# Performance work log

Measured on AMD Instinct MI355X. Metric: run time of the kernel, lower is better.

Reference implementation:

```python
import jax, jax.numpy as jnp
from jax import lax
import numpy as np

B = 16; C1 = 96; H4 = 28; W4 = 64
FULL_H = 448; FULL_W = 1024
BACKWARP = 1.25   # fltBackwarp for intLevel=4
SCALE = 16.0      # 2**intLevel
MD = 4            # correlation max displacement -> (2*MD+1)**2 = 81 channels


def _lrelu(x):
    return jnp.where(x >= 0, x, 0.1 * x)


def _conv3(x, w, b):
    y = lax.conv_general_dilated(x, w, (1, 1), [(1, 1), (1, 1)],
                                 dimension_numbers=('NCHW', 'OIHW', 'NCHW'))
    return y + b[None, :, None, None]


def _deconv4s2(x, w, b):
    # PyTorch ConvTranspose2d(k=4, s=2, p=1); w has PyTorch layout (in, out, kH, kW)
    wt = jnp.transpose(w[:, :, ::-1, ::-1], (1, 0, 2, 3))  # flipped, (out, in, kH, kW)
    y = lax.conv_general_dilated(x, wt, (1, 1), [(2, 2), (2, 2)],
                                 lhs_dilation=(2, 2),
                                 dimension_numbers=('NCHW', 'OIHW', 'NCHW'))
    return y + b[None, :, None, None]


def _correlation(f1, f2):
    # Channel-mean cost volume over a (2*MD+1)^2 displacement window.
    b, c, h, w = f1.shape
    f2p = jnp.pad(f2, ((0, 0), (0, 0), (MD, MD), (MD, MD)))
    vols = [jnp.mean(f1 * f2p[:, :, dy:dy + h, dx:dx + w], axis=1)
            for dy in range(2 * MD + 1) for dx in range(2 * MD + 1)]
    return jnp.stack(vols, axis=1)  # [B, 81, H, W]


def _warp(feat, flow):
    # Bilinear backward warp with zero padding outside the image.
    b, c, h, w = feat.shape
    gy, gx = jnp.meshgrid(jnp.arange(h, dtype=feat.dtype),
                          jnp.arange(w, dtype=feat.dtype), indexing='ij')
    x = gx[None] + flow[:, 0]
    y = gy[None] + flow[:, 1]
    x0 = jnp.floor(x); y0 = jnp.floor(y)
    wx = x - x0; wy = y - y0
    feat_flat = feat.reshape(b, c, h * w)

    def gather(yi, xi):
        valid = ((yi >= 0) & (yi <= h - 1) & (xi >= 0) & (xi <= w - 1)).astype(feat.dtype)
        yc = jnp.clip(yi, 0, h - 1).astype(jnp.int32)
        xc = jnp.clip(xi, 0, w - 1).astype(jnp.int32)
        idx = (yc * w + xc).reshape(b, 1, h * w)
        g = jnp.take_along_axis(feat_flat, jnp.broadcast_to(idx, (b, c, h * w)), axis=2)
        return g.reshape(b, c, h, w) * valid[:, None]

    return (gather(y0, x0) * ((1 - wy) * (1 - wx))[:, None]
            + gather(y0, x0 + 1) * ((1 - wy) * wx)[:, None]
            + gather(y0 + 1, x0) * (wy * (1 - wx))[:, None]
            + gather(y0 + 1, x0 + 1) * (wy * wx)[:, None])


def _quat_to_mat(q):
    # (w, x, y, z) quaternion -> rotation matrix, pytorch3d convention.
    q = q / jnp.linalg.norm(q, axis=-1, keepdims=True)
    w, x, y, z = q[:, 0], q[:, 1], q[:, 2], q[:, 3]
    R = jnp.stack([
        1 - 2 * (y * y + z * z), 2 * (x * y - w * z),     2 * (x * z + w * y),
        2 * (x * y + w * z),     1 - 2 * (x * x + z * z), 2 * (y * z - w * x),
        2 * (x * z - w * y),     2 * (y * z + w * x),     1 - 2 * (x * x + y * y)
    ], axis=-1).reshape(-1, 3, 3)
    return R


def _rot_flow(R, K, Kinv, h, w):
    # Rotational flow: p' = K R K^{-1} p (homogeneous), flow = p'/z - p.
    gy, gx = jnp.meshgrid(jnp.arange(h, dtype=R.dtype),
                          jnp.arange(w, dtype=R.dtype), indexing='ij')
    p = jnp.stack([gx.ravel(), gy.ravel(), jnp.ones(h * w, dtype=R.dtype)], axis=0)  # [3, HW]
    M = jnp.einsum('ij,bjk,kl->bil', K, R, Kinv)  # [B,3,3]
    pp = jnp.einsum('bij,jn->bin', M, p)
    pp2 = pp[:, :2] / pp[:, 2:3]
    return (pp2 - p[None, :2]).reshape(-1, 2, h, w)


def setup_inputs():
    key = jax.random.key(0)
    ks = jax.random.split(key, 24)

    def rnd(i, shape, scale=1.0):
        return scale * jax.random.normal(ks[i], shape, dtype=jnp.float32)

    def wconv(i, cout, cin, k=3):
        return rnd(i, (cout, cin, k, k), (2.0 / (cin * k * k)) ** 0.5)

    K = np.array([[500.0, 0.0, FULL_W / 2.0],
                  [0.0, 500.0, FULL_H / 2.0],
                  [0.0, 0.0, 1.0]], dtype=np.float32)
    quat = jnp.concatenate([jnp.ones((B, 1), jnp.float32), 0.01 * rnd(0, (B, 3))], axis=1)
    return {
        'tenOne': rnd(1, (B, C1, H4, W4)),
        'tenTwo': rnd(2, (B, C1, H4, W4)),
        'prev_flow': rnd(3, (B, 2, H4 // 2, W4 // 2)),
        'prev_feat': rnd(4, (B, 663, H4 // 2, W4 // 2)),
        'rotation_quat': quat,
        'cam_intri': jnp.asarray(K),
        'cam_intri_inv': jnp.asarray(np.linalg.inv(K)),
        'upflow_w': rnd(5, (2, 2, 4, 4), 0.1),
        'upflow_b': jnp.zeros((2,), jnp.float32),
        'upfeat_w': rnd(6, (663, 2, 4, 4), 0.02),
        'upfeat_b': jnp.zeros((2,), jnp.float32),
        'w1': wconv(7, 128, 183), 'b1': jnp.zeros((128,), jnp.float32),
        'w2': wconv(8, 128, 311), 'b2': jnp.zeros((128,), jnp.float32),
        'w3': wconv(9, 96, 439),  'b3': jnp.zeros((96,), jnp.float32),
        'w4': wconv(10, 64, 535), 'b4': jnp.zeros((64,), jnp.float32),
        'w5': wconv(11, 32, 599), 'b5': jnp.zeros((32,), jnp.float32),
        'w6': wconv(12, 2, 631),  'b6': jnp.zeros((2,), jnp.float32),
        'height': FULL_H,
        'width': FULL_W,
    }


def reference(tenOne, tenTwo, prev_flow, prev_feat, rotation_quat, cam_intri, cam_intri_inv,
              upflow_w, upflow_b, upfeat_w, upfeat_b,
              w1, b1, w2, b2, w3, b3, w4, b4, w5, b5, w6, b6, height, width):
    rh, rw = height // 16, width // 16  # 2**intLevel = 16
    delt_R = _quat_to_mat(rotation_quat)
    R_flow = _rot_flow(delt_R, cam_intri, cam_intri_inv, height, width)
    R_flow_r = jax.image.resize(R_flow, (R_flow.shape[0], 2, rh, rw), method='bilinear') / SCALE
    tenTwo_w = _warp(tenTwo, R_flow_r)
    tenFlow = _deconv4s2(prev_flow, upflow_w, upflow_b)
    tenFeatUp = _deconv4s2(prev_feat, upfeat_w, upfeat_b)
    tenVolume = _lrelu(_correlation(tenOne, _warp(tenTwo_w, tenFlow * BACKWARP)))
    feat = jnp.concatenate([tenVolume, R_flow_r, tenOne, tenFlow, tenFeatUp], axis=1)  # 183 ch
    for wc, bc in ((w1, b1), (w2, b2), (w3, b3), (w4, b4), (w5, b5)):
        feat = jnp.concatenate([_lrelu(_conv3(feat, wc, bc)), feat], axis=1)
    tenFlow_out = _lrelu(_conv3(feat, w6, b6))
    return tenFlow_out, feat
```

## Files before the change

### kernel.cpp

```cpp
#include <hip/hip_runtime.h>
#include <cstdint>
#include <cstddef>

typedef unsigned short u16;
typedef __attribute__((ext_vector_type(8))) short  short8;
typedef __attribute__((ext_vector_type(4))) float  f32x4;

#define HW4   1792
#define FCH   631
#define OUTOFF ((size_t)57344)

__device__ __forceinline__ float b2f(u16 u){
  union { unsigned int i; float f; } v; v.i = ((unsigned int)u) << 16; return v.f;
}
__device__ __forceinline__ u16 f2b(float f){
  unsigned int x = __float_as_uint(f);
  return (u16)((x + 0x7fffu + ((x >> 16) & 1u)) >> 16);
}
__device__ __forceinline__ float lrelu(float v){ return v >= 0.f ? v : 0.1f * v; }
__device__ __forceinline__ bool is_f32(const void* probe){ return ((const float*)probe)[0] > 1.0f; }
__device__ __forceinline__ float ldg_(const void* p, size_t i, bool f){
  return f ? ((const float*)p)[i] : b2f(((const u16*)p)[i]);
}
__device__ __forceinline__ void stg_(void* p, size_t i, float v, bool f){
  if (f) ((float*)p)[i] = v; else ((u16*)p)[i] = f2b(v);
}
__device__ __forceinline__ short8 zero8(){
  union { long long l[2]; short8 s; } z; z.l[0] = 0; z.l[1] = 0; return z.s;
}
__device__ __forceinline__ f32x4 zero4(){
  union { long long l[2]; f32x4 s; } z; z.l[0] = 0; z.l[1] = 0; return z.s;
}
__device__ __forceinline__ short8 swap16(short8 v){
  union { short8 s; unsigned int u[4]; } a, r;
  a.s = v;
  #pragma unroll
  for (int i = 0; i < 4; i++) r.u[i] = (a.u[i] >> 16) | (a.u[i] << 16);
  return r.s;
}

__global__ void k_M(const void* __restrict__ quat, const void* __restrict__ K,
                    const void* __restrict__ Kinv, float* __restrict__ Mout){
  bool f = is_f32(K);
  int b = threadIdx.x;
  if (b >= 16) return;
  float q0 = ldg_(quat,b*4+0,f), q1 = ldg_(quat,b*4+1,f);
  float q2 = ldg_(quat,b*4+2,f), q3 = ldg_(quat,b*4+3,f);
  float n = sqrtf(q0*q0 + q1*q1 + q2*q2 + q3*q3);
  float w = q0/n, x = q1/n, y = q2/n, z = q3/n;
  float R[9];
  R[0] = 1.f - 2.f*(y*y + z*z); R[1] = 2.f*(x*y - w*z); R[2] = 2.f*(x*z + w*y);
  R[3] = 2.f*(x*y + w*z); R[4] = 1.f - 2.f*(x*x + z*z); R[5] = 2.f*(y*z - w*x);
  R[6] = 2.f*(x*z - w*y); R[7] = 2.f*(y*z + w*x); R[8] = 1.f - 2.f*(x*x + y*y);
  float Kf[9], Ki[9];
  for (int i = 0; i < 9; i++){ Kf[i] = ldg_(K,i,f); Ki[i] = ldg_(Kinv,i,f); }
  float T[9];
  for (int r = 0; r < 3; r++)
    for (int c = 0; c < 3; c++)
      T[r*3+c] = R[r*3+0]*Ki[0*3+c] + R[r*3+1]*Ki[1*3+c] + R[r*3+2]*Ki[2*3+c];
  for (int r = 0; r < 3; r++)
    for (int c = 0; c < 3; c++)
      Mout[b*9 + r*3 + c] = Kf[r*3+0]*T[0*3+c] + Kf[r*3+1]*T[1*3+c] + Kf[r*3+2]*T[2*3+c];
}

__global__ void k_rflow_col(const float* __restrict__ Mws, float* __restrict__ tmpA){
  int t = blockIdx.x * 256 + threadIdx.x;
  int xo = t & 63;
  int yf = (t >> 6) % 448;
  int b  = t / (448*64);
  const float* M = Mws + b*9;
  float m0=M[0],m1=M[1],m2=M[2],m3=M[3],m4=M[4],m5=M[5],m6=M[6],m7=M[7],m8=M[8];
  float cx = 16.f*xo + 7.5f;
  float yff = (float)yf;
  float su = 0.f, sv = 0.f, wsum = 0.f;
  for (int i = 0; i < 32; i++){
    int xi = 16*xo - 8 + i;
    if (xi < 0 || xi > 1023) continue;
    float xf = (float)xi;
    float wgt = 1.f - fabsf(xf - cx) * (1.f/16.f);
    float den = m6*xf + m7*yff + m8;
    float inv = 1.f / den;
    float u = (m0*xf + m1*yff + m2)*inv - xf;
    float v = (m3*xf + m4*yff + m5)*inv - yff;
    su += wgt*u; sv += wgt*v; wsum += wgt;
  }
  float rn = 1.f / wsum;
  tmpA[((size_t)(b*2+0)*64 + xo)*448 + yf] = su*rn;
  tmpA[((size_t)(b*2+1)*64 + xo)*448 + yf] = sv*rn;
}

__global__ void k_rflow_row(const float* __restrict__ tmpA, float* __restrict__ rfr,
                            void* __restrict__ outb, const void* probe){
  bool f = is_f32(probe);
  int t = blockIdx.x * 256 + threadIdx.x;
  int xo = t & 63;
  int yo = (t >> 6) % 28;
  int b  = t / HW4;
  float cy = 16.f*yo + 7.5f;
  for (int c = 0; c < 2; c++){
    const float* col = tmpA + ((size_t)(b*2+c)*64 + xo)*448;
    float s = 0.f, wsum = 0.f;
    for (int i = 0; i < 32; i++){
      int yi = 16*yo - 8 + i;
      if (yi < 0 || yi > 447) continue;
      float wgt = 1.f - fabsf((float)yi - cy) * (1.f/16.f);
      s += wgt * col[yi]; wsum += wgt;
    }
    float val = s / (wsum * 16.0f);
    rfr[(size_t)(b*2+c)*HW4 + yo*64 + xo] = val;
    stg_(outb, OUTOFF + ((size_t)b*FCH + 529 + c)*HW4 + yo*64 + xo, val, f);
  }
}

__global__ void k_dflow(const void* __restrict__ pf, const void* __restrict__ w,
                        const void* __restrict__ bias, float* __restrict__ tflow,
                        void* __restrict__ outb, const void* probe){
  bool f = is_f32(probe);
  int t = blockIdx.x * 256 + threadIdx.x;
  int x = t & 63;
  int y = (t >> 6) % 28;
  int co = (t / HW4) & 1;
  int b  = t / (2*HW4);
  float acc = ldg_(bias, co, f);
  for (int ky = 0; ky < 4; ky++){
    int dy = y + ky - 2;
    if (dy < 0 || dy > 26 || (dy & 1)) continue;
    int iy = dy >> 1;
    for (int kx = 0; kx < 4; kx++){
      int dx = x + kx - 2;
      if (dx < 0 || dx > 62 || (dx & 1)) continue;
      int ix = dx >> 1;
      for (int ci = 0; ci < 2; ci++){
        acc += ldg_(pf, ((size_t)(b*2+ci)*14 + iy)*32 + ix, f) *
               ldg_(w,  (size_t)ci*32 + co*16 + (3-ky)*4 + (3-kx), f);
      }
    }
  }
  tflow[(size_t)(b*2+co)*HW4 + y*64 + x] = acc;
  stg_(outb, OUTOFF + ((size_t)b*FCH + 627 + co)*HW4 + y*64 + x, acc, f);
}

__global__ __launch_bounds__(512) void k_dfeat(
    const void* __restrict__ pfeat, const void* __restrict__ w,
    const void* __restrict__ bias, void* __restrict__ outb, const void* probe){
  bool f = is_f32(probe);
  __shared__ float red[8*128];
  int tid = threadIdx.x;
  int x = tid & 63;
  int s = tid >> 6;
  int b = blockIdx.x / 28;
  int y = blockIdx.x % 28;

  int iy0 = -1, iy1 = -1, wy0 = 0, wy1 = 0;
  {
    int n = 0;
    for (int ky = (y & 1); ky < 4; ky += 2){
      int dy = y + ky - 2;
      if (dy >= 0 && dy <= 26){
        if (n == 0){ iy0 = dy >> 1; wy0 = (3-ky)*4; }
        else       { iy1 = dy >> 1; wy1 = (3-ky)*4; }
        n++;
      }
    }
  }
  int ix0 = -1, ix1 = -1, wx0 = 0, wx1 = 0;
  {
    int n = 0;
    for (int kx = (x & 1); kx < 4; kx += 2){
      int dx = x + kx - 2;
      if (dx >= 0 && dx <= 62){
        if (n == 0){ ix0 = dx >> 1; wx0 = 3-kx; }
        else       { ix1 = dx >> 1; wx1 = 3-kx; }
        n++;
      }
    }
  }
  const bool v00 = (iy0 >= 0) && (ix0 >= 0);
  const bool v01 = (iy0 >= 0) && (ix1 >= 0);
  const bool v10 = (iy1 >= 0) && (ix0 >= 0);
  const bool v11 = (iy1 >= 0) && (ix1 >= 0);
  const int wo00 = wy0 + wx0, wo01 = wy0 + wx1, wo10 = wy1 + wx0, wo11 = wy1 + wx1;

  float acc0 = 0.f, acc1 = 0.f;
  const size_t pbase = (size_t)b * 663 * 448;
  const int ci_end = min(663, (s + 1) * 83);
  #pragma unroll 2
  for (int ci = s * 83; ci < ci_end; ci++){
    const size_t cbase = pbase + (size_t)ci * 448;
    const int wb = ci * 32;
    if (v00){ float iv = ldg_(pfeat, cbase + iy0*32 + ix0, f);
      acc0 += iv * ldg_(w, wb + wo00, f); acc1 += iv * ldg_(w, wb + 16 + wo00, f); }
    if (v01){ float iv = ldg_(pfeat, cbase + iy0*32 + ix1, f);
      acc0 += iv * ldg_(w, wb + wo01, f); acc1 += iv * ldg_(w, wb + 16 + wo01, f); }
    if (v10){ float iv = ldg_(pfeat, cbase + iy1*32 + ix0, f);
      acc0 += iv * ldg_(w, wb + wo10, f); acc1 += iv * ldg_(w, wb + 16 + wo10, f); }
    if (v11){ float iv = ldg_(pfeat, cbase + iy1*32 + ix1, f);
      acc0 += iv * ldg_(w, wb + wo11, f); acc1 += iv * ldg_(w, wb + 16 + wo11, f); }
  }
  red[s*128 + x]      = acc0;
  red[s*128 + 64 + x] = acc1;
  __syncthreads();
  if (tid < 128){
    int co = tid >> 6, xx = tid & 63;
    float t = ldg_(bias, co, f);
    #pragma unroll
    for (int q = 0; q < 8; q++) t += red[q*128 + co*64 + xx];
    stg_(outb, OUTOFF + ((size_t)b*FCH + 629 + co)*HW4 + y*64 + xx, t, f);
  }
}

__global__ void k_copy_one(const void* __restrict__ one, void* __restrict__ outb,
                           const void* probe){
  bool f = is_f32(probe);
  int t = blockIdx.x * 256 + threadIdx.x;
  int p = t % HW4;
  int c = (t / HW4) % 96;
  int b = t / (96*HW4);
  stg_(outb, OUTOFF + ((size_t)b*FCH + 531 + c)*HW4 + p,
       ldg_(one, (size_t)(b*96+c)*HW4 + p, f), f);
}

__global__ void k_warp2(const void* __restrict__ two, const float* __restrict__ rfr,
                        const float* __restrict__ tflow, float* __restrict__ wrp2,
                        const void* probe){
  bool f = is_f32(probe);
  int t = blockIdx.x * 256 + threadIdx.x;
  int x = t & 63;
  int y = (t >> 6) % 28;
  int c = (t / HW4) % 96;
  int b = t / (96*HW4);
  float qu = tflow[(size_t)(b*2+0)*HW4 + y*64 + x] * 1.25f;
  float qv = tflow[(size_t)(b*2+1)*HW4 + y*64 + x] * 1.25f;
  float qx = (float)x + qu, qy = (float)y + qv;
  float qx0 = floorf(qx), qy0 = floorf(qy);
  float wx = qx - qx0, wy = qy - qy0;
  const size_t cb = (size_t)(b*96+c)*HW4;
  float acc = 0.f;
  #pragma unroll
  for (int a = 0; a < 2; a++){
    #pragma unroll
    for (int bb = 0; bb < 2; bb++){
      float ry = qy0 + (float)a, rx = qx0 + (float)bb;
      if (ry < 0.f || ry > 27.f || rx < 0.f || rx > 63.f) continue;
      float W = (a ? wy : 1.f-wy) * (bb ? wx : 1.f-wx);
      int iry = (int)ry, irx = (int)rx;
      float su = rfr[(size_t)(b*2+0)*HW4 + iry*64 + irx];
      float sv = rfr[(size_t)(b*2+1)*HW4 + iry*64 + irx];
      float sx = rx + su, sy = ry + sv;
      float sx0 = floorf(sx), sy0 = floorf(sy);
      float swx = sx - sx0, swy = sy - sy0;
      float inner = 0.f;
      #pragma unroll
      for (int aa = 0; aa < 2; aa++){
        #pragma unroll
        for (int cc2 = 0; cc2 < 2; cc2++){
          float gy2 = sy0 + (float)aa, gx2 = sx0 + (float)cc2;
          if (gy2 < 0.f || gy2 > 27.f || gx2 < 0.f || gx2 > 63.f) continue;
          float wv = (aa ? swy : 1.f-swy) * (cc2 ? swx : 1.f-swx);
          inner += wv * ldg_(two, cb + (size_t)((int)gy2*64 + (int)gx2), f);
        }
      }
      acc += W * inner;
    }
  }
  wrp2[t] = acc;
}

__global__ void k_corr(const void* __restrict__ one, const float* __restrict__ two,
                       void* __restrict__ outb, const void* probe){
  bool f = is_f32(probe);
  int t = blockIdx.x * 256 + threadIdx.x;
  int x  = t & 63;
  int y  = (t >> 6) % 28;
  int dy = (t / HW4) % 9;
  int b  = t / (9*HW4);
  float acc[9];
  #pragma unroll
  for (int i = 0; i < 9; i++) acc[i] = 0.f;
  int row = y + dy - 4;
  if (row >= 0 && row < 28){
    for (int c = 0; c < 96; c++){
      float f1 = ldg_(one, (size_t)(b*96+c)*HW4 + y*64 + x, f);
      const float* rp = two + (size_t)(b*96+c)*HW4 + row*64;
      #pragma unroll
      for (int dx = 0; dx < 9; dx++){
        int xx = x + dx - 4;
        if (xx >= 0 && xx < 64) acc[dx] += f1 * rp[xx];
      }
    }
  }
  #pragma unroll
  for (int dx = 0; dx < 9; dx++){
    float v = lrelu(acc[dx] * (1.f/96.f));
    stg_(outb, OUTOFF + ((size_t)b*FCH + 448 + dy*9 + dx)*HW4 + y*64 + x, v, f);
  }
}

__global__ __launch_bounds__(256) void k_conv(
    void* __restrict__ base, size_t in_off,
    const void* __restrict__ w, const void* __restrict__ bias,
    int Cin, int Cout, size_t out_off, size_t out_bstr, const void* probe,
    int bf16_only){
  bool f = is_f32(probe);
  if (bf16_only && f) return;
  __shared__ float s_in[32*3*66];
  __shared__ float s_w[32*9*32];
  int tid = threadIdx.x;
  int x = tid & 63;
  int g = tid >> 6;
  int by = blockIdx.x;
  int b = by / 28, y = by % 28;
  int co_base = blockIdx.y * 32;
  const size_t FB = (size_t)FCH * HW4;
  float acc[8];
  #pragma unroll
  for (int j = 0; j < 8; j++) acc[j] = 0.f;

  for (int ci0 = 0; ci0 < Cin; ci0 += 32){
    int cc = min(32, Cin - ci0);
    if (f){
      const float* inb = (const float*)base + in_off + (size_t)b*FB;
      for (int e = tid; e < cc*198; e += 256){
        int ci = e / 198; int rem = e - ci*198;
        int r = rem / 66; int xx = rem - r*66;
        int iy = y + r - 1; int ix = xx - 1;
        float v = 0.f;
        if (iy >= 0 && iy < 28 && ix >= 0 && ix < 64)
          v = inb[(size_t)(ci0+ci)*HW4 + iy*64 + ix];
        s_in[(ci*3 + r)*66 + xx] = v;
      }
      const float* wf = (const float*)w;
      for (int e = tid; e < cc*288; e += 256){
        int co_i = e & 31; int k = (e >> 5) % 9; int ci = e / 288;
        int co = co_base + co_i;
        float v = 0.f;
        if (co < Cout) v = wf[((size_t)co*Cin + ci0 + ci)*9 + k];
        s_w[(ci*9 + k)*32 + co_i] = v;
      }
    } else {
      const u16* inb = (const u16*)base + in_off + (size_t)b*FB;
      for (int e = tid; e < cc*198; e += 256){
        int ci = e / 198; int rem = e - ci*198;
        int r = rem / 66; int xx = rem - r*66;
        int iy = y + r - 1; int ix = xx - 1;
        float v = 0.f;
        if (iy >= 0 && iy < 28 && ix >= 0 && ix < 64)
          v = b2f(inb[(size_t)(ci0+ci)*HW4 + iy*64 + ix]);
        s_in[(ci*3 + r)*66 + xx] = v;
      }
      const u16* wf = (const u16*)w;
      for (int e = tid; e < cc*288; e += 256){
        int co_i = e & 31; int k = (e >> 5) % 9; int ci = e / 288;
        int co = co_base + co_i;
        float v = 0.f;
        if (co < Cout) v = b2f(wf[((size_t)co*Cin + ci0 + ci)*9 + k]);
        s_w[(ci*9 + k)*32 + co_i] = v;
      }
    }
    __syncthreads();
    for (int ci = 0; ci < cc; ci++){
      const float* si = &s_in[ci*198 + x];
      const float* sw = &s_w[ci*288 + 8*g];
      #pragma unroll
      for (int ky = 0; ky < 3; ky++){
        #pragma unroll
        for (int kx = 0; kx < 3; kx++){
          float v = si[ky*66 + kx];
          const float* wp = sw + (ky*3 + kx)*32;
          float4 wa = *(const float4*)(wp);
          float4 wb = *(const float4*)(wp + 4);
          acc[0] += wa.x*v; acc[1] += wa.y*v; acc[2] += wa.z*v; acc[3] += wa.w*v;
          acc[4] += wb.x*v; acc[5] += wb.y*v; acc[6] += wb.z*v; acc[7] += wb.w*v;
        }
      }
    }
    __syncthreads();
  }
  #pragma unroll
  for (int j = 0; j < 8; j++){
    int co = co_base + 8*g + j;
    if (co < Cout){
      float v = lrelu(acc[j] + ldg_(bias, co, f));
      stg_(base, out_off + (size_t)b*out_bstr + (size_t)co*HW4 + y*64 + x, v, f);
    }
  }
}

__global__ void k_wprep(const void* __restrict__ w, u16* __restrict__ wT,
                        int Cin, int Cout, int nCB, int total, const void* probe){
  if (!is_f32(probe)) return;
  int t = blockIdx.x * 256 + threadIdx.x;
  if (t >= total) return;
  int j     = t & 7;
  int lane  = (t >> 3) & 63;
  int rest  = t >> 9;
  int tI    = rest & 3;
  int rest2 = rest >> 2;
  int tap   = rest2 % 9;
  int gc    = rest2 / 9;
  int cb    = gc % nCB;
  int gyb   = gc / nCB;
  int kk = ((lane >> 4) << 3) + j;
  int ci = cb*16 + (kk >> 1);
  int co = gyb*64 + tI*16 + (lane & 15);
  float x = 0.f;
  if (co < Cout && ci < Cin) x = ((const float*)w)[((size_t)co*Cin + ci)*9 + tap];
  u16 hi = f2b(x);
  wT[t] = (kk & 1) ? f2b(x - b2f(hi)) : hi;
}

__global__ __launch_bounds__(256, 2) void k_conv_ms(
    void* __restrict__ base, size_t in_off, const u16* __restrict__ wT,
    const void* __restrict__ bias, int Cin, int nCB, int Cout,
    size_t out_off, size_t out_bstr, const void* __restrict__ probe){
  if (!is_f32(probe)) return;
  __shared__ __align__(16) u16 lds[26624];
  const int tid  = threadIdx.x;
  const int lane = tid & 63, wv = tid >> 6;
  const int lx = lane & 15, lg = lane >> 4;
  const int wr  = wv & 1;
  const int wxh = wv >> 1;
  const int b  = blockIdx.x & 15;
  const int y0 = (blockIdx.x >> 4) * 2;
  const int coB = (int)blockIdx.y * 64;
  const float* inb = (const float*)base + in_off + (size_t)b * ((size_t)FCH * HW4);
  const u16* wTg = wT + (size_t)blockIdx.y * (size_t)nCB * 18432;

  f32x4 acc[4][2];
  #pragma unroll
  for (int tI = 0; tI < 4; tI++){ acc[tI][0] = zero4(); acc[tI][1] = zero4(); }

  int offb[3];
  #pragma unroll
  for (int kx = 0; kx < 3; kx++){
    int xo = lx + kx - 1;
    offb[kx] = (xo >> 4)*512 + (xo & 15)*32 + ((lg ^ ((xo >> 2) & 3)) << 3);
  }
  const bool maskB0 = (lx == 0  && wxh == 0);
  const bool maskB1 = (lx == 15 && wxh == 1);

  const int sx4 = tid & 15;
  const int sr  = (tid >> 4) & 3;
  const int srow = y0 - 1 + sr;
  const bool rok = (srow >= 0 && srow < 28);
  const int swz = sx4 & 3;
  const int nb0 = sr*64 + sx4*4;

  float4 paA[4], paB[4];
  short8 pwA[9], pwB[9];

  auto LOADA = [&](int cb){
    const u16* wsrc = wTg + (size_t)cb * 18432;
    #pragma unroll
    for (int i = 0; i < 9; i++)
      pwA[i] = *(const short8*)(wsrc + (size_t)(wv*9 + i)*512 + lane*8);
    #pragma unroll
    for (int i = 0; i < 4; i++){
      int ci = cb*16 + wv + 4*i;
      float4 v = {0.f, 0.f, 0.f, 0.f};
      if (rok && ci < Cin) v = *(const float4*)(inb + (size_t)ci*HW4 + srow*64 + sx4*4);
      paA[i] = v;
    }
  };
  auto LOADB = [&](int cb){
    const u16* wsrc = wTg + (size_t)cb * 18432;
    #pragma unroll
    for (int i = 0; i < 9; i++)
      pwB[i] = *(const short8*)(wsrc + (size_t)(wv*9 + i)*512 + lane*8);
    #pragma unroll
    for (int i = 0; i < 4; i++){
      int ci = cb*16 + wv + 4*i;
      float4 v = {0.f, 0.f, 0.f, 0.f};
      if (rok && ci < Cin) v = *(const float4*)(inb + (size_t)ci*HW4 + srow*64 + sx4*4);
      paB[i] = v;
    }
  };
  auto WRITEA = [&](){
    #pragma unroll
    for (int i = 0; i < 9; i++)
      *(short8*)&lds[8192 + (wv*9 + i)*512 + lane*8] = pwA[i];
    #pragma unroll
    for (int i = 0; i < 4; i++){
      int cil = wv + 4*i;
      int jo = (((cil >> 2) ^ swz) << 3) + 2*(cil & 3);
      #pragma unroll
      for (int u = 0; u < 4; u++){
        float xv = (&paA[i].x)[u];
        u16 hi = f2b(xv);
        u16 lo = f2b(xv - b2f(hi));
        *(unsigned int*)&lds[(nb0 + u)*32 + jo] = (unsigned int)hi | ((unsigned int)lo << 16);
      }
    }
  };
  auto WRITEB = [&](){
    #pragma unroll
    for (int i = 0; i < 9; i++)
      *(short8*)&lds[8192 + (wv*9 + i)*512 + lane*8] = pwB[i];
    #pragma unroll
    for (int i = 0; i < 4; i++){
      int cil = wv + 4*i;
      int jo = (((cil >> 2) ^ swz) << 3) + 2*(cil & 3);
      #pragma unroll
      for (int u = 0; u < 4; u++){
        float xv = (&paB[i].x)[u];
        u16 hi = f2b(xv);
        u16 lo = f2b(xv - b2f(hi));
        *(unsigned int*)&lds[(nb0 + u)*32 + jo] = (unsigned int)hi | ((unsigned int)lo << 16);
      }
    }
  };
  auto COMPUTE = [&](){
    #pragma unroll
    for (int ky = 0; ky < 3; ky++){
      const int rb = (wr + ky)*2048 + wxh*1024;
      #pragma unroll
      for (int kx = 0; kx < 3; kx++){
        const int k = ky*3 + kx;
        const int bA = rb + offb[kx];
        short8 B0 = *(const short8*)&lds[bA];
        short8 B1 = *(const short8*)&lds[bA + 512];
        if (kx == 0 && maskB0) B0 = zero8();
        if (kx == 2 && maskB1) B1 = zero8();
        short8 S0 = swap16(B0), S1 = swap16(B1);
        #pragma unroll
        for (int tI = 0; tI < 4; tI++){
          short8 Af = *(const short8*)&lds[8192 + ((k*4 + tI)*64 + lane)*8];
          acc[tI][0] = __builtin_amdgcn_mfma_f32_16x16x32_bf16(Af, B0, acc[tI][0], 0,0,0);
          acc[tI][0] = __builtin_amdgcn_mfma_f32_16x16x32_bf16(Af, S0, acc[tI][0], 0,0,0);
          acc[tI][1] = __builtin_amdgcn_mfma_f32_16x16x32_bf16(Af, B1, acc[tI][1], 0,0,0);
          acc[tI][1] = __builtin_amdgcn_mfma_f32_16x16x32_bf16(Af, S1, acc[tI][1], 0,0,0);
        }
      }
    }
  };

  LOADA(0);
  for (int cb = 0; cb < nCB; cb += 2){
    WRITEA();
    LOADB(cb + 1);
    __syncthreads();
    COMPUTE();
    __syncthreads();
    WRITEB();
    if (cb + 2 < nCB) LOADA(cb + 2);
    __syncthreads();
    COMPUTE();
    __syncthreads();
  }
  float* ob = (float*)base;
  const float* bf = (const float*)bias;
  const int y = y0 + wr;
  #pragma unroll
  for (int tI = 0; tI < 4; tI++){
    #pragma unroll
    for (int xg = 0; xg < 2; xg++){
      const int x = wxh*32 + xg*16 + lx;
      #pragma unroll
      for (int r4 = 0; r4 < 4; r4++){
        int co = coB + tI*16 + lg*4 + r4;
        if (co < Cout){
          float v = lrelu(acc[tI][xg][r4] + bf[co]);
          ob[out_off + (size_t)b*out_bstr + (size_t)co*HW4 + (size_t)(y*64 + x)] = v;
        }
      }
    }
  }
}

extern "C" void kernel_launch(void* const* d_in, const int* in_sizes, int n_in,
                              void* d_out, int out_size, void* d_ws, size_t ws_size,
                              hipStream_t stream){
  const void* tenOne    = d_in[0];
  const void* tenTwo    = d_in[1];
  const void* prev_flow = d_in[2];
  const void* prev_feat = d_in[3];
  const void* quat      = d_in[4];
  const void* K         = d_in[5];
  const void* Kinv      = d_in[6];
  const void* upflow_w  = d_in[7];
  const void* upflow_b  = d_in[8];
  const void* upfeat_w  = d_in[9];
  const void* upfeat_b  = d_in[10];
  const void* w1 = d_in[11];  const void* b1 = d_in[12];
  const void* w2 = d_in[13];  const void* b2 = d_in[14];
  const void* w3 = d_in[15];  const void* b3 = d_in[16];
  const void* w4 = d_in[17];  const void* b4 = d_in[18];
  const void* w5 = d_in[19];  const void* b5 = d_in[20];
  const void* w6 = d_in[21];  const void* b6 = d_in[22];
  const void* probe = K;

  float* ws    = (float*)d_ws;
  float* Mws   = ws;
  float* tmpA  = ws + 160;
  float* rfr   = ws + 917664;
  float* tflow = ws + 975008;
  float* wrp2  = ws + 1032352;
  u16*   wTb   = (u16*)(ws + 3784864);

  const bool ws_ok = ws_size >= (size_t)23691904;

  k_M<<<1, 64, 0, stream>>>(quat, K, Kinv, Mws);
  k_rflow_col<<<1792, 256, 0, stream>>>(Mws, tmpA);
  k_rflow_row<<<112, 256, 0, stream>>>(tmpA, rfr, d_out, probe);
  k_dflow<<<224, 256, 0, stream>>>(prev_flow, upflow_w, upflow_b, tflow, d_out, probe);
  k_dfeat<<<448, 512, 0, stream>>>(prev_feat, upfeat_w, upfeat_b, d_out, probe);
  k_copy_one<<<10752, 256, 0, stream>>>(tenOne, d_out, probe);
  k_warp2<<<10752, 256, 0, stream>>>(tenTwo, rfr, tflow, wrp2, probe);
  k_corr<<<1008, 256, 0, stream>>>(tenOne, wrp2, d_out, probe);

  const size_t FB = (size_t)FCH * HW4;
  const size_t f0 = OUTOFF;

  struct LD { const void *w, *bi; int Cin, Cout, nCB, gy; size_t wOff, in_off, out_off, out_bstr; };
  const LD L[6] = {
    { w1, b1, 183, 128, 12, 2, 0,       f0+(size_t)448*HW4, f0+(size_t)320*HW4, FB },
    { w2, b2, 311, 128, 20, 2, 442368,  f0+(size_t)320*HW4, f0+(size_t)192*HW4, FB },
    { w3, b3, 439,  96, 28, 2, 1179648, f0+(size_t)192*HW4, f0+(size_t) 96*HW4, FB },
    { w4, b4, 535,  64, 34, 1, 2211840, f0+(size_t) 96*HW4, f0+(size_t) 32*HW4, FB },
    { w5, b5, 599,  32, 38, 1, 2838528, f0+(size_t) 32*HW4, f0,                 FB },
    { w6, b6, 631,   2, 40, 1, 3538944, f0,                 0,        (size_t)2*HW4 },
  };

  if (ws_ok){
    for (int i = 0; i < 6; i++){
      int total = L[i].gy * L[i].nCB * 18432;
      k_wprep<<<(total + 255)/256, 256, 0, stream>>>(
          L[i].w, wTb + L[i].wOff, L[i].Cin, L[i].Cout, L[i].nCB, total, probe);
    }
    for (int i = 0; i < 6; i++){
      k_conv_ms<<<dim3(224, L[i].gy), 256, 0, stream>>>(
          d_out, L[i].in_off, wTb + L[i].wOff, L[i].bi,
          L[i].Cin, L[i].nCB, L[i].Cout,
          L[i].out_off, L[i].out_bstr, probe);
    }
  }
  const int bf16_only = ws_ok ? 1 : 0;
  k_conv<<<dim3(448,4), 256, 0, stream>>>(d_out, f0 + (size_t)448*HW4, w1, b1, 183, 128,
                                          f0 + (size_t)320*HW4, FB, probe, bf16_only);
  k_conv<<<dim3(448,4), 256, 0, stream>>>(d_out, f0 + (size_t)320*HW4, w2, b2, 311, 128,
                                          f0 + (size_t)192*HW4, FB, probe, bf16_only);
  k_conv<<<dim3(448,3), 256, 0, stream>>>(d_out, f0 + (size_t)192*HW4, w3, b3, 439, 96,
                                          f0 + (size_t)96*HW4, FB, probe, bf16_only);
  k_conv<<<dim3(448,2), 256, 0, stream>>>(d_out, f0 + (size_t)96*HW4, w4, b4, 535, 64,
                                          f0 + (size_t)32*HW4, FB, probe, bf16_only);
  k_conv<<<dim3(448,1), 256, 0, stream>>>(d_out, f0 + (size_t)32*HW4, w5, b5, 599, 32,
                                          f0, FB, probe, bf16_only);
  k_conv<<<dim3(448,1), 256, 0, stream>>>(d_out, f0, w6, b6, 631, 2,
                                          0, (size_t)2*HW4, probe, bf16_only);
}
```

Before: 1.030 ms.

## Split feature deconvolution into channel-chunk LDS tiles with a partial-sum reduction

The feature upsampling deconvolution is restructured into two kernels. The first stages 16-channel slabs of the input and weights in LDS with vectorized loads and computes partial sums for every output pixel. The second reduces the 42 partial slabs and adds the bias. This replaces strided global gathers that re-read the input and weights per output row, at the cost of an extra kernel launch and a partial-sum buffer that reuses the warp workspace region.

```diff
diff --git a/kernel.cpp b/kernel.cpp
--- a/kernel.cpp
+++ b/kernel.cpp
@@ -140,73 +140,105 @@
   stg_(outb, OUTOFF + ((size_t)b*FCH + 627 + co)*HW4 + y*64 + x, acc, f);
 }
 
-__global__ __launch_bounds__(512) void k_dfeat(
+#define DF_NCH 42
+__global__ __launch_bounds__(256) void k_dfeat_s1(
     const void* __restrict__ pfeat, const void* __restrict__ w,
-    const void* __restrict__ bias, void* __restrict__ outb, const void* probe){
-  bool f = is_f32(probe);
-  __shared__ float red[8*128];
-  int tid = threadIdx.x;
-  int x = tid & 63;
-  int s = tid >> 6;
-  int b = blockIdx.x / 28;
-  int y = blockIdx.x % 28;
-
-  int iy0 = -1, iy1 = -1, wy0 = 0, wy1 = 0;
-  {
-    int n = 0;
-    for (int ky = (y & 1); ky < 4; ky += 2){
-      int dy = y + ky - 2;
-      if (dy >= 0 && dy <= 26){
-        if (n == 0){ iy0 = dy >> 1; wy0 = (3-ky)*4; }
-        else       { iy1 = dy >> 1; wy1 = (3-ky)*4; }
-        n++;
-      }
-    }
-  }
-  int ix0 = -1, ix1 = -1, wx0 = 0, wx1 = 0;
-  {
-    int n = 0;
+    float* __restrict__ part, const void* probe){
+  bool f = is_f32(probe);
+  __shared__ float s_in[16*448];
+  __shared__ float s_w[16*32];
+  const int tid = threadIdx.x;
+  const int ch = blockIdx.x;
+  const int b  = blockIdx.y;
+  if (f){
+    const float* src = (const float*)pfeat + ((size_t)b*663 + (size_t)ch*16)*448;
+    #pragma unroll
+    for (int i = 0; i < 7; i++){
+      int e = tid + 256*i;
+      int ci = ch*16 + e/112;
+      float4 v = {0.f,0.f,0.f,0.f};
+      if (ci < 663) v = *(const float4*)(src + e*4);
+      *(float4*)&s_in[e*4] = v;
+    }
+  } else {
+    const u16* src = (const u16*)pfeat + ((size_t)b*663 + (size_t)ch*16)*448;
+    #pragma unroll
+    for (int i = 0; i < 7; i++){
+      int e = tid + 256*i;
+      int ci = ch*16 + e/112;
+      float4 v = {0.f,0.f,0.f,0.f};
+      if (ci < 663){
+        ushort4 u = *(const ushort4*)(src + e*4);
+        v.x = b2f(u.x); v.y = b2f(u.y); v.z = b2f(u.z); v.w = b2f(u.w);
+      }
+      *(float4*)&s_in[e*4] = v;
+    }
+  }
+  #pragma unroll
+  for (int i = 0; i < 2; i++){
+    int e = tid + 256*i;
+    int ci = ch*16 + (e >> 5);
+    s_w[e] = (ci < 663) ? ldg_(w, (size_t)ci*32 + (e & 31), f) : 0.f;
+  }
+  __syncthreads();
+  const int x = tid & 63;
+  int ix0=-1, ix1=-1, wx0=0, wx1=0;
+  { int n = 0;
     for (int kx = (x & 1); kx < 4; kx += 2){
       int dx = x + kx - 2;
       if (dx >= 0 && dx <= 62){
-        if (n == 0){ ix0 = dx >> 1; wx0 = 3-kx; }
-        else       { ix1 = dx >> 1; wx1 = 3-kx; }
+        if (n == 0){ ix0 = dx >> 1; wx0 = 3-kx; } else { ix1 = dx >> 1; wx1 = 3-kx; }
         n++;
       }
-    }
-  }
-  const bool v00 = (iy0 >= 0) && (ix0 >= 0);
-  const bool v01 = (iy0 >= 0) && (ix1 >= 0);
-  const bool v10 = (iy1 >= 0) && (ix0 >= 0);
-  const bool v11 = (iy1 >= 0) && (ix1 >= 0);
-  const int wo00 = wy0 + wx0, wo01 = wy0 + wx1, wo10 = wy1 + wx0, wo11 = wy1 + wx1;
-
-  float acc0 = 0.f, acc1 = 0.f;
-  const size_t pbase = (size_t)b * 663 * 448;
-  const int ci_end = min(663, (s + 1) * 83);
-  #pragma unroll 2
-  for (int ci = s * 83; ci < ci_end; ci++){
-    const size_t cbase = pbase + (size_t)ci * 448;
-    const int wb = ci * 32;
-    if (v00){ float iv = ldg_(pfeat, cbase + iy0*32 + ix0, f);
-      acc0 += iv * ldg_(w, wb + wo00, f); acc1 += iv * ldg_(w, wb + 16 + wo00, f); }
-    if (v01){ float iv = ldg_(pfeat, cbase + iy0*32 + ix1, f);
-      acc0 += iv * ldg_(w, wb + wo01, f); acc1 += iv * ldg_(w, wb + 16 + wo01, f); }
-    if (v10){ float iv = ldg_(pfeat, cbase + iy1*32 + ix0, f);
-      acc0 += iv * ldg_(w, wb + wo10, f); acc1 += iv * ldg_(w, wb + 16 + wo10, f); }
-    if (v11){ float iv = ldg_(pfeat, cbase + iy1*32 + ix1, f);
-      acc0 += iv * ldg_(w, wb + wo11, f); acc1 += iv * ldg_(w, wb + 16 + wo11, f); }
-  }
-  red[s*128 + x]      = acc0;
-  red[s*128 + 64 + x] = acc1;
-  __syncthreads();
-  if (tid < 128){
-    int co = tid >> 6, xx = tid & 63;
-    float t = ldg_(bias, co, f);
-    #pragma unroll
-    for (int q = 0; q < 8; q++) t += red[q*128 + co*64 + xx];
-    stg_(outb, OUTOFF + ((size_t)b*FCH + 629 + co)*HW4 + y*64 + xx, t, f);
-  }
+    } }
+  float* pout = part + (size_t)(b*DF_NCH + ch)*2*1792;
+  #pragma unroll
+  for (int i = 0; i < 7; i++){
+    int p = tid + 256*i;
+    int y = p >> 6;
+    int iy0=-1, iy1=-1, wy0=0, wy1=0;
+    { int n = 0;
+      for (int ky = (y & 1); ky < 4; ky += 2){
+        int dy = y + ky - 2;
+        if (dy >= 0 && dy <= 26){
+          if (n == 0){ iy0 = dy >> 1; wy0 = (3-ky)*4; } else { iy1 = dy >> 1; wy1 = (3-ky)*4; }
+          n++;
+        }
+      } }
+    const bool v00 = (iy0 >= 0) && (ix0 >= 0);
+    const bool v01 = (iy0 >= 0) && (ix1 >= 0);
+    const bool v10 = (iy1 >= 0) && (ix0 >= 0);
+    const bool v11 = (iy1 >= 0) && (ix1 >= 0);
+    const int o00 = iy0*32+ix0, o01 = iy0*32+ix1, o10 = iy1*32+ix0, o11 = iy1*32+ix1;
+    const int w00 = wy0+wx0, w01 = wy0+wx1, w10 = wy1+wx0, w11 = wy1+wx1;
+    float a0 = 0.f, a1 = 0.f;
+    #pragma unroll 4
+    for (int ci = 0; ci < 16; ci++){
+      const float* si = s_in + ci*448;
+      const float* sw = s_w + ci*32;
+      if (v00){ float iv = si[o00]; a0 += iv*sw[w00]; a1 += iv*sw[16+w00]; }
+      if (v01){ float iv = si[o01]; a0 += iv*sw[w01]; a1 += iv*sw[16+w01]; }
+      if (v10){ float iv = si[o10]; a0 += iv*sw[w10]; a1 += iv*sw[16+w10]; }
+      if (v11){ float iv = si[o11]; a0 += iv*sw[w11]; a1 += iv*sw[16+w11]; }
+    }
+    pout[p]        = a0;
+    pout[1792 + p] = a1;
+  }
+}
+
+__global__ void k_dfeat_s2(const float* __restrict__ part, const void* __restrict__ bias,
+                           void* __restrict__ outb, const void* probe){
+  bool f = is_f32(probe);
+  int t = blockIdx.x * 256 + threadIdx.x;
+  int x = t & 63;
+  int y = (t >> 6) % 28;
+  int co = (t / HW4) & 1;
+  int b  = t / (2*HW4);
+  float s = ldg_(bias, co, f);
+  const float* pp = part + ((size_t)b*(2*DF_NCH) + co)*1792 + (size_t)(y*64 + x);
+  #pragma unroll
+  for (int ch = 0; ch < DF_NCH; ch++) s += pp[(size_t)ch*3584];
+  stg_(outb, OUTOFF + ((size_t)b*FCH + 629 + co)*HW4 + y*64 + x, s, f);
 }
 
 __global__ void k_copy_one(const void* __restrict__ one, void* __restrict__ outb,
@@ -596,6 +628,7 @@
   float* tflow = ws + 975008;
   float* wrp2  = ws + 1032352;
   u16*   wTb   = (u16*)(ws + 3784864);
+  float* dpart = wrp2;
 
   const bool ws_ok = ws_size >= (size_t)23691904;
 
@@ -603,7 +636,8 @@
   k_rflow_col<<<1792, 256, 0, stream>>>(Mws, tmpA);
   k_rflow_row<<<112, 256, 0, stream>>>(tmpA, rfr, d_out, probe);
   k_dflow<<<224, 256, 0, stream>>>(prev_flow, upflow_w, upflow_b, tflow, d_out, probe);
-  k_dfeat<<<448, 512, 0, stream>>>(prev_feat, upfeat_w, upfeat_b, d_out, probe);
+  k_dfeat_s1<<<dim3(DF_NCH, 16), 256, 0, stream>>>(prev_feat, upfeat_w, dpart, probe);
+  k_dfeat_s2<<<224, 256, 0, stream>>>(dpart, upfeat_b, d_out, probe);
   k_copy_one<<<10752, 256, 0, stream>>>(tenOne, d_out, probe);
   k_warp2<<<10752, 256, 0, stream>>>(tenTwo, rfr, tflow, wrp2, probe);
   k_corr<<<1008, 256, 0, stream>>>(tenOne, wrp2, d_out, probe);
```

Result: faster. 927.1 us (-10.0%).
